# Kernel tuning notes

Hardware: AMD Instinct MI355X
Metric: run time of the kernel (lower is better)

## Reference

```python
import jax, jax.numpy as jnp
import numpy as np

HIDDEN_DIM = 64
MEMORY_SLOTS = 4
SEQ_LEN = 24
VOCAB_SIZE = 64
B = 65536


def setup_inputs() -> dict:
    key = jax.random.key(0)
    ks = jax.random.split(key, 16)
    s = 0.05
    inp = {
        "seqs": jax.random.randint(ks[0], (B, SEQ_LEN), 0, VOCAB_SIZE + 2),
        "query_tok": jax.random.randint(ks[1], (B,), 0, VOCAB_SIZE + 2),
        # embedding table [VOCAB+2, H]
        "embed": jax.random.normal(ks[2], (VOCAB_SIZE + 2, HIDDEN_DIM), jnp.float32) * s,
        # joint_net: Linear(H + S*H -> H), ReLU, Linear(H -> H), ReLU  (weights stored [in, out])
        "W1": jax.random.normal(ks[3], (HIDDEN_DIM + MEMORY_SLOTS * HIDDEN_DIM, HIDDEN_DIM), jnp.float32) * s,
        "b1": jax.random.normal(ks[4], (HIDDEN_DIM,), jnp.float32) * s,
        "W2": jax.random.normal(ks[5], (HIDDEN_DIM, HIDDEN_DIM), jnp.float32) * s,
        "b2": jax.random.normal(ks[6], (HIDDEN_DIM,), jnp.float32) * s,
        # write_head: Linear(H -> H)
        "Ww": jax.random.normal(ks[7], (HIDDEN_DIM, HIDDEN_DIM), jnp.float32) * s,
        "bw": jax.random.normal(ks[8], (HIDDEN_DIM,), jnp.float32) * s,
        # evict_head: Linear(H -> MEMORY_SLOTS)
        "We": jax.random.normal(ks[9], (HIDDEN_DIM, MEMORY_SLOTS), jnp.float32) * s,
        "be": jax.random.normal(ks[10], (MEMORY_SLOTS,), jnp.float32) * s,
        # read_head: Linear(2H -> H), ReLU, Linear(H -> VOCAB)
        "Wr1": jax.random.normal(ks[11], (2 * HIDDEN_DIM, HIDDEN_DIM), jnp.float32) * s,
        "br1": jax.random.normal(ks[12], (HIDDEN_DIM,), jnp.float32) * s,
        "Wr2": jax.random.normal(ks[13], (HIDDEN_DIM, VOCAB_SIZE), jnp.float32) * s,
        "br2": jax.random.normal(ks[14], (VOCAB_SIZE,), jnp.float32) * s,
    }
    return inp


def reference(seqs, query_tok, embed, W1, b1, W2, b2, Ww, bw, We, be, Wr1, br1, Wr2, br2):
    # Token embeddings for the first SEQ_LEN-1 positions, scanned over time: [T, B, H]
    emb_seq = jnp.swapaxes(embed[seqs[:, : SEQ_LEN - 1]], 0, 1)

    def step(mem, emb_t):  # mem: [B, S, H], emb_t: [B, H]
        joint_in = jnp.concatenate([emb_t, mem.reshape(mem.shape[0], -1)], axis=-1)  # [B, H + S*H]
        h = jax.nn.relu(joint_in @ W1 + b1)
        h = jax.nn.relu(h @ W2 + b2)                      # [B, H]
        write_vec = h @ Ww + bw                           # [B, H]
        evict_logits = h @ We + be                        # [B, S]
        evict_idx = jnp.argmax(evict_logits, axis=-1)     # [B] hard, non-diff
        mask = jax.nn.one_hot(evict_idx, MEMORY_SLOTS, dtype=bool)[..., None]  # [B, S, 1]
        new_mem = jnp.where(mask, write_vec[:, None, :], mem)
        return new_mem, None

    mem0 = jnp.zeros((seqs.shape[0], MEMORY_SLOTS, HIDDEN_DIM), jnp.float32)
    mem, _ = jax.lax.scan(step, mem0, emb_seq)

    mem_summary = mem.mean(axis=1)                        # [B, H]
    q_emb = embed[query_tok]                              # [B, H]
    r = jnp.concatenate([q_emb, mem_summary], axis=-1)    # [B, 2H]
    logits = jax.nn.relu(r @ Wr1 + br1) @ Wr2 + br2       # [B, VOCAB]
    return logits
```

## Files before the change

### kernel.cpp

```cpp
#include <hip/hip_runtime.h>

#define H       64
#define NSLOT   4
#define NSTEP   23
#define NB      65536
#define NV      66
#define SEQL    24
#define LPE     8
#define TPB     512
#define EPB     128
#define ACTSTR  68
#define MROW    68
#define JL      40
#define MSSTR   (JL * MROW + 4)

#define OFF_EW1   0
#define OFF_EWR1  (NV * H)
#define OFF_M     (2 * NV * H)
#define OFF_PB    (OFF_M + NSLOT * H * H)
#define OFF_HL    (OFF_PB + NSLOT * H)

__global__ __launch_bounds__(256) void k_setup_tables(
    const float* __restrict__ embed, const float* __restrict__ W1, const float* __restrict__ b1,
    const float* __restrict__ Wr1, const float* __restrict__ br1, float* __restrict__ ws)
{
    int idx = blockIdx.x * 256 + threadIdx.x;
    if (idx >= NV * H) return;
    int t = idx >> 6, k = idx & 63;
    float a1 = b1[k], a2 = br1[k];
    for (int j = 0; j < H; ++j) {
        float e = embed[t * H + j];
        a1 = fmaf(e, W1[j * H + k], a1);
        a2 = fmaf(e, Wr1[j * H + k], a2);
    }
    ws[OFF_EW1 + idx]  = a1;
    ws[OFF_EWR1 + idx] = a2;
}

__global__ __launch_bounds__(256) void k_setup_fuse(
    const float* __restrict__ W1, const float* __restrict__ Ww, const float* __restrict__ bw,
    float* __restrict__ ws)
{
    int idx = blockIdx.x * 256 + threadIdx.x;
    if (idx < NSLOT * H * H) {
        int s = idx >> 12, j = (idx >> 6) & 63, k = idx & 63;
        const float* w1s = W1 + (size_t)(H + s * H) * H;
        float acc = 0.f;
        for (int p = 0; p < H; ++p)
            acc = fmaf(Ww[j * H + p], w1s[p * H + k], acc);
        ws[OFF_M + idx] = acc;
    } else if (idx < NSLOT * H * H + NSLOT * H) {
        int r = idx - NSLOT * H * H;
        int s = r >> 6, k = r & 63;
        const float* w1s = W1 + (size_t)(H + s * H) * H;
        float acc = 0.f;
        for (int p = 0; p < H; ++p)
            acc = fmaf(bw[p], w1s[p * H + k], acc);
        ws[OFF_PB + r] = acc;
    }
}

#define FMA8V(w0, w1, a, ACC) do {                                          \
    ACC[0]=fmaf((a),w0.x,ACC[0]); ACC[1]=fmaf((a),w0.y,ACC[1]);            \
    ACC[2]=fmaf((a),w0.z,ACC[2]); ACC[3]=fmaf((a),w0.w,ACC[3]);            \
    ACC[4]=fmaf((a),w1.x,ACC[4]); ACC[5]=fmaf((a),w1.y,ACC[5]);            \
    ACC[6]=fmaf((a),w1.z,ACC[6]); ACC[7]=fmaf((a),w1.w,ACC[7]);            \
} while (0)

#define LOAD8(ptr, A) do {                                                  \
    const float4* _b = (const float4*)(ptr);                                \
    float4 _b0 = _b[0], _b1 = _b[1];                                        \
    A[0]=_b0.x; A[1]=_b0.y; A[2]=_b0.z; A[3]=_b0.w;                        \
    A[4]=_b1.x; A[5]=_b1.y; A[6]=_b1.z; A[7]=_b1.w;                        \
} while (0)

#define STORE8(rowptr, A) do {                                              \
    float4* _d = (float4*)(rowptr);                                         \
    _d[0] = make_float4(A[0], A[1], A[2], A[3]);                            \
    _d[1] = make_float4(A[4], A[5], A[6], A[7]);                            \
} while (0)

__global__ __launch_bounds__(TPB, 2) void k_main(
    const float* __restrict__ W2, const float* __restrict__ b2,
    const float* __restrict__ Ww, const float* __restrict__ bw,
    const float* __restrict__ We, const float* __restrict__ be,
    const float* __restrict__ Wr1, const float* __restrict__ Wr2, const float* __restrict__ br2,
    const int* __restrict__ qtok, const int* __restrict__ seqs,
    const float* __restrict__ ws, float* hl, float* __restrict__ out)
{
    __shared__ float sM[NSLOT * MSSTR];
    __shared__ float sAct[EPB * ACTSTR];
    __shared__ float sPb[NSLOT * 68];
    __shared__ float sWeS[8 * 36];

    const int tid  = threadIdx.x;
    const int m    = tid & (LPE - 1);
    const int g    = tid >> 3;
    const int eA   = g;
    const int eB   = g + 64;
    const int gidA = blockIdx.x * EPB + eA;
    const int gidB = blockIdx.x * EPB + eB;
    const int k0   = m * 8;

    if (tid < 256) {
        int s = tid >> 6, j = tid & 63;
        if (j < JL) {
            const float4* src = (const float4*)(ws + OFF_M + (size_t)(s * H + j) * H);
            float4* dst = (float4*)(sM + s * MSSTR + j * MROW);
#pragma unroll
            for (int k = 0; k < 16; ++k) dst[k] = src[k];
        }
    }
    if (tid >= 256 && tid < 512) {
        int r = tid - 256;
        int s = r >> 6, k = r & 63;
        sPb[s * 68 + k] = ws[OFF_PB + s * H + k];
    }
    if (tid < 256) {
        int mm = tid >> 5, rem = tid & 31;
        sWeS[mm * 36 + rem] = We[tid];
    }
    __syncthreads();

    const float* embW1b  = ws + OFF_EW1;
    const float* embWr1b = ws + OFF_EWR1;
    const float* Mg      = ws + OFF_M;
    float* hlA = hl + (size_t)gidA * (NSLOT * H) + k0;
    float* hlB = hl + (size_t)gidB * (NSLOT * H) + k0;

    float pA0[8], pA1[8], pA2[8], pA3[8], cA[8];
    float pB0[8], pB1[8], pB2[8], pB3[8], cB[8];
#pragma unroll
    for (int i = 0; i < 8; ++i) {
        pA0[i]=0.f; pA1[i]=0.f; pA2[i]=0.f; pA3[i]=0.f; cA[i]=0.f;
        pB0[i]=0.f; pB1[i]=0.f; pB2[i]=0.f; pB3[i]=0.f; cB[i]=0.f;
    }
    int maskA = 0, maskB = 0;

    float b2r[8];
    LOAD8(b2 + k0, b2r);
    const float4 be4 = *(const float4*)be;

    int tokA = seqs[gidA * SEQL];
    int tokB = seqs[gidB * SEQL];

    float accA[8], accB[8];
    float* rowA = sAct + eA * ACTSTR;
    float* rowB = sAct + eB * ACTSTR;

#pragma unroll 1
    for (int t = 0; t < NSTEP; ++t) {
        int tokAn = seqs[gidA * SEQL + t + 1];
        int tokBn = seqs[gidB * SEQL + t + 1];

        {
            float hA[8], hB[8];
            LOAD8(embW1b + tokA * H + k0, hA);
            LOAD8(embW1b + tokB * H + k0, hB);
#pragma unroll
            for (int i = 0; i < 8; ++i) {
                hA[i] = fmaxf(hA[i] + cA[i], 0.f);
                hB[i] = fmaxf(hB[i] + cB[i], 0.f);
            }
            STORE8(rowA + k0, hA);
            STORE8(rowB + k0, hB);
        }

#pragma unroll
        for (int i = 0; i < 8; ++i) { accA[i] = b2r[i]; accB[i] = b2r[i]; }
#pragma unroll 4
        for (int jq = 0; jq < 16; ++jq) {
            float4 a4 = *(const float4*)(rowA + jq * 4);
            float4 b4 = *(const float4*)(rowB + jq * 4);
            float aAv[4] = {a4.x, a4.y, a4.z, a4.w};
            float aBv[4] = {b4.x, b4.y, b4.z, b4.w};
#pragma unroll
            for (int jj = 0; jj < 4; ++jj) {
                const float4* w = (const float4*)(W2 + (jq * 4 + jj) * H + k0);
                float4 w0 = w[0], w1 = w[1];
                FMA8V(w0, w1, aAv[jj], accA);
                FMA8V(w0, w1, aBv[jj], accB);
            }
        }
        float h2A[8], h2B[8];
#pragma unroll
        for (int i = 0; i < 8; ++i) {
            h2A[i] = fmaxf(accA[i], 0.f);
            h2B[i] = fmaxf(accB[i], 0.f);
        }
        STORE8(rowA + k0, h2A);
        STORE8(rowB + k0, h2B);

        float lA0 = 0.f, lA1 = 0.f, lA2 = 0.f, lA3 = 0.f;
        float lB0 = 0.f, lB1 = 0.f, lB2 = 0.f, lB3 = 0.f;
        {
            const float* wsl = sWeS + m * 36;
#pragma unroll
            for (int i = 0; i < 8; ++i) {
                float4 we4 = *(const float4*)(wsl + i * 4);
                lA0 = fmaf(h2A[i], we4.x, lA0); lA1 = fmaf(h2A[i], we4.y, lA1);
                lA2 = fmaf(h2A[i], we4.z, lA2); lA3 = fmaf(h2A[i], we4.w, lA3);
                lB0 = fmaf(h2B[i], we4.x, lB0); lB1 = fmaf(h2B[i], we4.y, lB1);
                lB2 = fmaf(h2B[i], we4.z, lB2); lB3 = fmaf(h2B[i], we4.w, lB3);
            }
        }
#pragma unroll
        for (int d = 1; d <= 4; d <<= 1) {
            lA0 += __shfl_xor(lA0, d); lA1 += __shfl_xor(lA1, d);
            lA2 += __shfl_xor(lA2, d); lA3 += __shfl_xor(lA3, d);
            lB0 += __shfl_xor(lB0, d); lB1 += __shfl_xor(lB1, d);
            lB2 += __shfl_xor(lB2, d); lB3 += __shfl_xor(lB3, d);
        }
        lA0 += be4.x; lA1 += be4.y; lA2 += be4.z; lA3 += be4.w;
        lB0 += be4.x; lB1 += be4.y; lB2 += be4.z; lB3 += be4.w;

        int eSA = 0; float bstA = lA0;
        if (lA1 > bstA) { bstA = lA1; eSA = 1; }
        if (lA2 > bstA) { bstA = lA2; eSA = 2; }
        if (lA3 > bstA) { bstA = lA3; eSA = 3; }
        int eSB = 0; float bstB = lB0;
        if (lB1 > bstB) { bstB = lB1; eSB = 1; }
        if (lB2 > bstB) { bstB = lB2; eSB = 2; }
        if (lB3 > bstB) { bstB = lB3; eSB = 3; }

        bool a0 = (eSA == 0), a1 = (eSA == 1), a2 = (eSA == 2), a3 = (eSA == 3);
        bool b0 = (eSB == 0), b1 = (eSB == 1), b2_ = (eSB == 2), b3 = (eSB == 3);

        STORE8(hlA + eSA * H, h2A);
        STORE8(hlB + eSB * H, h2B);
        maskA |= (1 << eSA);
        maskB |= (1 << eSB);

        LOAD8(sPb + eSA * 68 + k0, accA);
        LOAD8(sPb + eSB * 68 + k0, accB);
        const float* lMA = sM + eSA * MSSTR + k0;
        const float* lMB = sM + eSB * MSSTR + k0;
#pragma unroll 4
        for (int jq = 0; jq < JL / 4; ++jq) {
            float4 a4 = *(const float4*)(rowA + jq * 4);
            float4 b4 = *(const float4*)(rowB + jq * 4);
            float dAv[4] = {a4.x, a4.y, a4.z, a4.w};
            float dBv[4] = {b4.x, b4.y, b4.z, b4.w};
#pragma unroll
            for (int jj = 0; jj < 4; ++jj) {
                int j = jq * 4 + jj;
                const float4* wa = (const float4*)(lMA + j * MROW);
                const float4* wb = (const float4*)(lMB + j * MROW);
                float4 wa0 = wa[0], wa1 = wa[1];
                float4 wb0 = wb[0], wb1 = wb[1];
                FMA8V(wa0, wa1, dAv[jj], accA);
                FMA8V(wb0, wb1, dBv[jj], accB);
            }
        }
        {
            const float* gMA = Mg + (size_t)(eSA * H + JL) * H + k0;
            const float* gMB = Mg + (size_t)(eSB * H + JL) * H + k0;
#pragma unroll 2
            for (int jq = JL / 4; jq < 16; ++jq) {
                float4 a4 = *(const float4*)(rowA + jq * 4);
                float4 b4 = *(const float4*)(rowB + jq * 4);
                float dAv[4] = {a4.x, a4.y, a4.z, a4.w};
                float dBv[4] = {b4.x, b4.y, b4.z, b4.w};
#pragma unroll
                for (int jj = 0; jj < 4; ++jj) {
                    int jr = (jq * 4 + jj) - JL;
                    const float4* wa = (const float4*)(gMA + jr * H);
                    const float4* wb = (const float4*)(gMB + jr * H);
                    float4 wa0 = wa[0], wa1 = wa[1];
                    float4 wb0 = wb[0], wb1 = wb[1];
                    FMA8V(wa0, wa1, dAv[jj], accA);
                    FMA8V(wb0, wb1, dBv[jj], accB);
                }
            }
        }

#pragma unroll
        for (int i = 0; i < 8; ++i) {
            float pvA = accA[i], pvB = accB[i];
            float oldA = a0 ? pA0[i] : a1 ? pA1[i] : a2 ? pA2[i] : pA3[i];
            float oldB = b0 ? pB0[i] : b1 ? pB1[i] : b2_ ? pB2[i] : pB3[i];
            cA[i] += pvA - oldA;
            cB[i] += pvB - oldB;
            pA0[i] = a0 ? pvA : pA0[i];  pA1[i] = a1 ? pvA : pA1[i];
            pA2[i] = a2 ? pvA : pA2[i];  pA3[i] = a3 ? pvA : pA3[i];
            pB0[i] = b0 ? pvB : pB0[i];  pB1[i] = b1 ? pvB : pB1[i];
            pB2[i] = b2_ ? pvB : pB2[i]; pB3[i] = b3 ? pvB : pB3[i];
        }

        tokA = tokAn; tokB = tokBn;
    }

    __threadfence();
    {
        float hsA[8] = {0,0,0,0,0,0,0,0}, hsB[8] = {0,0,0,0,0,0,0,0};
#pragma unroll
        for (int s = 0; s < NSLOT; ++s) {
            float vA[8], vB[8];
            LOAD8(hlA + s * H, vA);
            LOAD8(hlB + s * H, vB);
            float fA = ((maskA >> s) & 1) ? 1.f : 0.f;
            float fB = ((maskB >> s) & 1) ? 1.f : 0.f;
#pragma unroll
            for (int i = 0; i < 8; ++i) {
                hsA[i] = fmaf(fA, vA[i], hsA[i]);
                hsB[i] = fmaf(fB, vB[i], hsB[i]);
            }
        }
        STORE8(rowA + k0, hsA);
        STORE8(rowB + k0, hsB);
    }

    {
        float bwr[8];
        LOAD8(bw + k0, bwr);
        float cntA = (float)__popc(maskA), cntB = (float)__popc(maskB);
#pragma unroll
        for (int i = 0; i < 8; ++i) { accA[i] = cntA * bwr[i]; accB[i] = cntB * bwr[i]; }
    }
#pragma unroll 4
    for (int jq = 0; jq < 16; ++jq) {
        float4 a4 = *(const float4*)(rowA + jq * 4);
        float4 b4 = *(const float4*)(rowB + jq * 4);
        float aAv[4] = {a4.x, a4.y, a4.z, a4.w};
        float aBv[4] = {b4.x, b4.y, b4.z, b4.w};
#pragma unroll
        for (int jj = 0; jj < 4; ++jj) {
            const float4* w = (const float4*)(Ww + (jq * 4 + jj) * H + k0);
            float4 w0 = w[0], w1 = w[1];
            FMA8V(w0, w1, aAv[jj], accA);
            FMA8V(w0, w1, aBv[jj], accB);
        }
    }
    {
        float msA[8], msB[8];
#pragma unroll
        for (int i = 0; i < 8; ++i) {
            msA[i] = accA[i] * 0.25f;
            msB[i] = accB[i] * 0.25f;
        }
        STORE8(rowA + k0, msA);
        STORE8(rowB + k0, msB);
    }

    int qA = qtok[gidA], qB = qtok[gidB];
    LOAD8(embWr1b + qA * H + k0, accA);
    LOAD8(embWr1b + qB * H + k0, accB);
#pragma unroll 4
    for (int jq = 0; jq < 16; ++jq) {
        float4 a4 = *(const float4*)(rowA + jq * 4);
        float4 b4 = *(const float4*)(rowB + jq * 4);
        float aAv[4] = {a4.x, a4.y, a4.z, a4.w};
        float aBv[4] = {b4.x, b4.y, b4.z, b4.w};
#pragma unroll
        for (int jj = 0; jj < 4; ++jj) {
            const float4* w = (const float4*)(Wr1 + (H + jq * 4 + jj) * H + k0);
            float4 w0 = w[0], w1 = w[1];
            FMA8V(w0, w1, aAv[jj], accA);
            FMA8V(w0, w1, aBv[jj], accB);
        }
    }
    {
        float rA[8], rB[8];
#pragma unroll
        for (int i = 0; i < 8; ++i) {
            rA[i] = fmaxf(accA[i], 0.f);
            rB[i] = fmaxf(accB[i], 0.f);
        }
        STORE8(rowA + k0, rA);
        STORE8(rowB + k0, rB);
    }

    LOAD8(br2 + k0, accA);
#pragma unroll
    for (int i = 0; i < 8; ++i) accB[i] = accA[i];
#pragma unroll 4
    for (int jq = 0; jq < 16; ++jq) {
        float4 a4 = *(const float4*)(rowA + jq * 4);
        float4 b4 = *(const float4*)(rowB + jq * 4);
        float aAv[4] = {a4.x, a4.y, a4.z, a4.w};
        float aBv[4] = {b4.x, b4.y, b4.z, b4.w};
#pragma unroll
        for (int jj = 0; jj < 4; ++jj) {
            const float4* w = (const float4*)(Wr2 + (jq * 4 + jj) * H + k0);
            float4 w0 = w[0], w1 = w[1];
            FMA8V(w0, w1, aAv[jj], accA);
            FMA8V(w0, w1, aBv[jj], accB);
        }
    }

    float4* oA = (float4*)(out + (size_t)gidA * H + k0);
    oA[0] = make_float4(accA[0], accA[1], accA[2], accA[3]);
    oA[1] = make_float4(accA[4], accA[5], accA[6], accA[7]);
    float4* oB = (float4*)(out + (size_t)gidB * H + k0);
    oB[0] = make_float4(accB[0], accB[1], accB[2], accB[3]);
    oB[1] = make_float4(accB[4], accB[5], accB[6], accB[7]);
}

extern "C" void kernel_launch(void* const* d_in, const int* in_sizes, int n_in,
                              void* d_out, int out_size, void* d_ws, size_t ws_size,
                              hipStream_t stream)
{
    const int*   seqs  = (const int*)d_in[0];
    const int*   qtok  = (const int*)d_in[1];
    const float* embed = (const float*)d_in[2];
    const float* W1    = (const float*)d_in[3];
    const float* b1    = (const float*)d_in[4];
    const float* W2    = (const float*)d_in[5];
    const float* b2    = (const float*)d_in[6];
    const float* Ww    = (const float*)d_in[7];
    const float* bw    = (const float*)d_in[8];
    const float* We    = (const float*)d_in[9];
    const float* be    = (const float*)d_in[10];
    const float* Wr1   = (const float*)d_in[11];
    const float* br1   = (const float*)d_in[12];
    const float* Wr2   = (const float*)d_in[13];
    const float* br2   = (const float*)d_in[14];
    float* out = (float*)d_out;
    float* ws  = (float*)d_ws;

    hipLaunchKernelGGL(k_setup_tables, dim3((NV * H + 255) / 256), dim3(256), 0, stream,
                       embed, W1, b1, Wr1, br1, ws);
    hipLaunchKernelGGL(k_setup_fuse, dim3((NSLOT * H * H + NSLOT * H + 255) / 256), dim3(256),
                       0, stream, W1, Ww, bw, ws);
    hipLaunchKernelGGL(k_main, dim3(NB / EPB), dim3(TPB), 0, stream,
                       W2, b2, Ww, bw, We, be, Wr1, Wr2, br2, qtok, seqs,
                       ws, ws + OFF_HL, out);
}
```

Baseline: 917.4 us.

## Process one element per thread group instead of two and cache more M rows

Each 8-lane group now handles a single batch element instead of two, halving per-thread register state (slot projections, accumulators) and the per-block element count. The freed LDS budget lets more rows of the precomputed slot matrix (48 instead of 40) live in shared memory, reducing global reads in the inner projection. The cost is that W2/M weight loads are no longer amortized across two elements, and the grid must double in block count.

```diff
diff --git a/kernel.cpp b/kernel.cpp
--- a/kernel.cpp
+++ b/kernel.cpp
@@ -8,11 +8,12 @@
 #define SEQL    24
 #define LPE     8
 #define TPB     512
-#define EPB     128
+#define EPB     64
 #define ACTSTR  68
 #define MROW    68
-#define JL      40
+#define JL      48
 #define MSSTR   (JL * MROW + 4)
+
 
 #define OFF_EW1   0
 #define OFF_EWR1  (NV * H)
@@ -97,9 +98,7 @@
     const int m    = tid & (LPE - 1);
     const int g    = tid >> 3;
     const int eA   = g;
-    const int eB   = g + 64;
     const int gidA = blockIdx.x * EPB + eA;
-    const int gidB = blockIdx.x * EPB + eB;
     const int k0   = m * 8;
 
     if (tid < 256) {
@@ -126,73 +125,56 @@
     const float* embWr1b = ws + OFF_EWR1;
     const float* Mg      = ws + OFF_M;
     float* hlA = hl + (size_t)gidA * (NSLOT * H) + k0;
-    float* hlB = hl + (size_t)gidB * (NSLOT * H) + k0;
 
     float pA0[8], pA1[8], pA2[8], pA3[8], cA[8];
-    float pB0[8], pB1[8], pB2[8], pB3[8], cB[8];
 #pragma unroll
     for (int i = 0; i < 8; ++i) {
         pA0[i]=0.f; pA1[i]=0.f; pA2[i]=0.f; pA3[i]=0.f; cA[i]=0.f;
-        pB0[i]=0.f; pB1[i]=0.f; pB2[i]=0.f; pB3[i]=0.f; cB[i]=0.f;
-    }
-    int maskA = 0, maskB = 0;
+    }
+    int maskA = 0;
 
     float b2r[8];
     LOAD8(b2 + k0, b2r);
     const float4 be4 = *(const float4*)be;
 
     int tokA = seqs[gidA * SEQL];
-    int tokB = seqs[gidB * SEQL];
-
-    float accA[8], accB[8];
+
+    float accA[8];
     float* rowA = sAct + eA * ACTSTR;
-    float* rowB = sAct + eB * ACTSTR;
 
 #pragma unroll 1
     for (int t = 0; t < NSTEP; ++t) {
         int tokAn = seqs[gidA * SEQL + t + 1];
-        int tokBn = seqs[gidB * SEQL + t + 1];
 
         {
-            float hA[8], hB[8];
+            float hA[8];
             LOAD8(embW1b + tokA * H + k0, hA);
-            LOAD8(embW1b + tokB * H + k0, hB);
-#pragma unroll
-            for (int i = 0; i < 8; ++i) {
+#pragma unroll
+            for (int i = 0; i < 8; ++i)
                 hA[i] = fmaxf(hA[i] + cA[i], 0.f);
-                hB[i] = fmaxf(hB[i] + cB[i], 0.f);
-            }
             STORE8(rowA + k0, hA);
-            STORE8(rowB + k0, hB);
-        }
-
-#pragma unroll
-        for (int i = 0; i < 8; ++i) { accA[i] = b2r[i]; accB[i] = b2r[i]; }
+        }
+
+#pragma unroll
+        for (int i = 0; i < 8; ++i) accA[i] = b2r[i];
 #pragma unroll 4
         for (int jq = 0; jq < 16; ++jq) {
             float4 a4 = *(const float4*)(rowA + jq * 4);
-            float4 b4 = *(const float4*)(rowB + jq * 4);
             float aAv[4] = {a4.x, a4.y, a4.z, a4.w};
-            float aBv[4] = {b4.x, b4.y, b4.z, b4.w};
 #pragma unroll
             for (int jj = 0; jj < 4; ++jj) {
                 const float4* w = (const float4*)(W2 + (jq * 4 + jj) * H + k0);
                 float4 w0 = w[0], w1 = w[1];
                 FMA8V(w0, w1, aAv[jj], accA);
-                FMA8V(w0, w1, aBv[jj], accB);
             }
         }
-        float h2A[8], h2B[8];
-#pragma unroll
-        for (int i = 0; i < 8; ++i) {
+        float h2A[8];
+#pragma unroll
+        for (int i = 0; i < 8; ++i)
             h2A[i] = fmaxf(accA[i], 0.f);
-            h2B[i] = fmaxf(accB[i], 0.f);
-        }
         STORE8(rowA + k0, h2A);
-        STORE8(rowB + k0, h2B);
 
         float lA0 = 0.f, lA1 = 0.f, lA2 = 0.f, lA3 = 0.f;
-        float lB0 = 0.f, lB1 = 0.f, lB2 = 0.f, lB3 = 0.f;
         {
             const float* wsl = sWeS + m * 36;
 #pragma unroll
@@ -200,200 +182,145 @@
                 float4 we4 = *(const float4*)(wsl + i * 4);
                 lA0 = fmaf(h2A[i], we4.x, lA0); lA1 = fmaf(h2A[i], we4.y, lA1);
                 lA2 = fmaf(h2A[i], we4.z, lA2); lA3 = fmaf(h2A[i], we4.w, lA3);
-                lB0 = fmaf(h2B[i], we4.x, lB0); lB1 = fmaf(h2B[i], we4.y, lB1);
-                lB2 = fmaf(h2B[i], we4.z, lB2); lB3 = fmaf(h2B[i], we4.w, lB3);
             }
         }
 #pragma unroll
         for (int d = 1; d <= 4; d <<= 1) {
             lA0 += __shfl_xor(lA0, d); lA1 += __shfl_xor(lA1, d);
             lA2 += __shfl_xor(lA2, d); lA3 += __shfl_xor(lA3, d);
-            lB0 += __shfl_xor(lB0, d); lB1 += __shfl_xor(lB1, d);
-            lB2 += __shfl_xor(lB2, d); lB3 += __shfl_xor(lB3, d);
         }
         lA0 += be4.x; lA1 += be4.y; lA2 += be4.z; lA3 += be4.w;
-        lB0 += be4.x; lB1 += be4.y; lB2 += be4.z; lB3 += be4.w;
 
         int eSA = 0; float bstA = lA0;
         if (lA1 > bstA) { bstA = lA1; eSA = 1; }
         if (lA2 > bstA) { bstA = lA2; eSA = 2; }
         if (lA3 > bstA) { bstA = lA3; eSA = 3; }
-        int eSB = 0; float bstB = lB0;
-        if (lB1 > bstB) { bstB = lB1; eSB = 1; }
-        if (lB2 > bstB) { bstB = lB2; eSB = 2; }
-        if (lB3 > bstB) { bstB = lB3; eSB = 3; }
 
         bool a0 = (eSA == 0), a1 = (eSA == 1), a2 = (eSA == 2), a3 = (eSA == 3);
-        bool b0 = (eSB == 0), b1 = (eSB == 1), b2_ = (eSB == 2), b3 = (eSB == 3);
 
         STORE8(hlA + eSA * H, h2A);
-        STORE8(hlB + eSB * H, h2B);
         maskA |= (1 << eSA);
-        maskB |= (1 << eSB);
 
         LOAD8(sPb + eSA * 68 + k0, accA);
-        LOAD8(sPb + eSB * 68 + k0, accB);
         const float* lMA = sM + eSA * MSSTR + k0;
-        const float* lMB = sM + eSB * MSSTR + k0;
 #pragma unroll 4
         for (int jq = 0; jq < JL / 4; ++jq) {
             float4 a4 = *(const float4*)(rowA + jq * 4);
-            float4 b4 = *(const float4*)(rowB + jq * 4);
             float dAv[4] = {a4.x, a4.y, a4.z, a4.w};
-            float dBv[4] = {b4.x, b4.y, b4.z, b4.w};
 #pragma unroll
             for (int jj = 0; jj < 4; ++jj) {
                 int j = jq * 4 + jj;
                 const float4* wa = (const float4*)(lMA + j * MROW);
-                const float4* wb = (const float4*)(lMB + j * MROW);
                 float4 wa0 = wa[0], wa1 = wa[1];
-                float4 wb0 = wb[0], wb1 = wb[1];
                 FMA8V(wa0, wa1, dAv[jj], accA);
-                FMA8V(wb0, wb1, dBv[jj], accB);
             }
         }
         {
             const float* gMA = Mg + (size_t)(eSA * H + JL) * H + k0;
-            const float* gMB = Mg + (size_t)(eSB * H + JL) * H + k0;
 #pragma unroll 2
             for (int jq = JL / 4; jq < 16; ++jq) {
                 float4 a4 = *(const float4*)(rowA + jq * 4);
-                float4 b4 = *(const float4*)(rowB + jq * 4);
                 float dAv[4] = {a4.x, a4.y, a4.z, a4.w};
-                float dBv[4] = {b4.x, b4.y, b4.z, b4.w};
 #pragma unroll
                 for (int jj = 0; jj < 4; ++jj) {
                     int jr = (jq * 4 + jj) - JL;
                     const float4* wa = (const float4*)(gMA + jr * H);
-                    const float4* wb = (const float4*)(gMB + jr * H);
                     float4 wa0 = wa[0], wa1 = wa[1];
-                    float4 wb0 = wb[0], wb1 = wb[1];
                     FMA8V(wa0, wa1, dAv[jj], accA);
-                    FMA8V(wb0, wb1, dBv[jj], accB);
                 }
             }
         }
 
 #pragma unroll
         for (int i = 0; i < 8; ++i) {
-            float pvA = accA[i], pvB = accB[i];
+            float pvA = accA[i];
             float oldA = a0 ? pA0[i] : a1 ? pA1[i] : a2 ? pA2[i] : pA3[i];
-            float oldB = b0 ? pB0[i] : b1 ? pB1[i] : b2_ ? pB2[i] : pB3[i];
             cA[i] += pvA - oldA;
-            cB[i] += pvB - oldB;
             pA0[i] = a0 ? pvA : pA0[i];  pA1[i] = a1 ? pvA : pA1[i];
             pA2[i] = a2 ? pvA : pA2[i];  pA3[i] = a3 ? pvA : pA3[i];
-            pB0[i] = b0 ? pvB : pB0[i];  pB1[i] = b1 ? pvB : pB1[i];
-            pB2[i] = b2_ ? pvB : pB2[i]; pB3[i] = b3 ? pvB : pB3[i];
-        }
-
-        tokA = tokAn; tokB = tokBn;
+        }
+
+        tokA = tokAn;
     }
 
     __threadfence();
     {
-        float hsA[8] = {0,0,0,0,0,0,0,0}, hsB[8] = {0,0,0,0,0,0,0,0};
+        float hsA[8] = {0,0,0,0,0,0,0,0};
 #pragma unroll
         for (int s = 0; s < NSLOT; ++s) {
-            float vA[8], vB[8];
+            float vA[8];
             LOAD8(hlA + s * H, vA);
-            LOAD8(hlB + s * H, vB);
             float fA = ((maskA >> s) & 1) ? 1.f : 0.f;
-            float fB = ((maskB >> s) & 1) ? 1.f : 0.f;
-#pragma unroll
-            for (int i = 0; i < 8; ++i) {
+#pragma unroll
+            for (int i = 0; i < 8; ++i)
                 hsA[i] = fmaf(fA, vA[i], hsA[i]);
-                hsB[i] = fmaf(fB, vB[i], hsB[i]);
-            }
         }
         STORE8(rowA + k0, hsA);
-        STORE8(rowB + k0, hsB);
     }
 
     {
         float bwr[8];
         LOAD8(bw + k0, bwr);
-        float cntA = (float)__popc(maskA), cntB = (float)__popc(maskB);
-#pragma unroll
-        for (int i = 0; i < 8; ++i) { accA[i] = cntA * bwr[i]; accB[i] = cntB * bwr[i]; }
+        float cntA = (float)__popc(maskA);
+#pragma unroll
+        for (int i = 0; i < 8; ++i) accA[i] = cntA * bwr[i];
     }
 #pragma unroll 4
     for (int jq = 0; jq < 16; ++jq) {
         float4 a4 = *(const float4*)(rowA + jq * 4);
-        float4 b4 = *(const float4*)(rowB + jq * 4);
         float aAv[4] = {a4.x, a4.y, a4.z, a4.w};
-        float aBv[4] = {b4.x, b4.y, b4.z, b4.w};
 #pragma unroll
         for (int jj = 0; jj < 4; ++jj) {
             const float4* w = (const float4*)(Ww + (jq * 4 + jj) * H + k0);
             float4 w0 = w[0], w1 = w[1];
             FMA8V(w0, w1, aAv[jj], accA);
-            FMA8V(w0, w1, aBv[jj], accB);
         }
     }
     {
-        float msA[8], msB[8];
-#pragma unroll
-        for (int i = 0; i < 8; ++i) {
+        float msA[8];
+#pragma unroll
+        for (int i = 0; i < 8; ++i)
             msA[i] = accA[i] * 0.25f;
-            msB[i] = accB[i] * 0.25f;
-        }
         STORE8(rowA + k0, msA);
-        STORE8(rowB + k0, msB);
-    }
-
-    int qA = qtok[gidA], qB = qtok[gidB];
+    }
+
+    int qA = qtok[gidA];
     LOAD8(embWr1b + qA * H + k0, accA);
-    LOAD8(embWr1b + qB * H + k0, accB);
 #pragma unroll 4
     for (int jq = 0; jq < 16; ++jq) {
         float4 a4 = *(const float4*)(rowA + jq * 4);
-        float4 b4 = *(const float4*)(rowB + jq * 4);
         float aAv[4] = {a4.x, a4.y, a4.z, a4.w};
-        float aBv[4] = {b4.x, b4.y, b4.z, b4.w};
 #pragma unroll
         for (int jj = 0; jj < 4; ++jj) {
             const float4* w = (const float4*)(Wr1 + (H + jq * 4 + jj) * H + k0);
             float4 w0 = w[0], w1 = w[1];
             FMA8V(w0, w1, aAv[jj], accA);
-            FMA8V(w0, w1, aBv[jj], accB);
         }
     }
     {
-        float rA[8], rB[8];
-#pragma unroll
-        for (int i = 0; i < 8; ++i) {
+        float rA[8];
+#pragma unroll
+        for (int i = 0; i < 8; ++i)
             rA[i] = fmaxf(accA[i], 0.f);
-            rB[i] = fmaxf(accB[i], 0.f);
-        }
         STORE8(rowA + k0, rA);
-        STORE8(rowB + k0, rB);
     }
 
     LOAD8(br2 + k0, accA);
-#pragma unroll
-    for (int i = 0; i < 8; ++i) accB[i] = accA[i];
 #pragma unroll 4
     for (int jq = 0; jq < 16; ++jq) {
         float4 a4 = *(const float4*)(rowA + jq * 4);
-        float4 b4 = *(const float4*)(rowB + jq * 4);
         float aAv[4] = {a4.x, a4.y, a4.z, a4.w};
-        float aBv[4] = {b4.x, b4.y, b4.z, b4.w};
 #pragma unroll
         for (int jj = 0; jj < 4; ++jj) {
             const float4* w = (const float4*)(Wr2 + (jq * 4 + jj) * H + k0);
             float4 w0 = w[0], w1 = w[1];
             FMA8V(w0, w1, aAv[jj], accA);
-            FMA8V(w0, w1, aBv[jj], accB);
         }
     }
 
     float4* oA = (float4*)(out + (size_t)gidA * H + k0);
     oA[0] = make_float4(accA[0], accA[1], accA[2], accA[3]);
     oA[1] = make_float4(accA[4], accA[5], accA[6], accA[7]);
-    float4* oB = (float4*)(out + (size_t)gidB * H + k0);
-    oB[0] = make_float4(accB[0], accB[1], accB[2], accB[3]);
-    oB[1] = make_float4(accB[4], accB[5], accB[6], accB[7]);
 }
 
 extern "C" void kernel_launch(void* const* d_in, const int* in_sizes, int n_in,
```

Result: slower. 1.255 ms (+36.8%).
